# Performance work log

Measured on AMD Instinct MI355X. Metric: run time of the kernel, lower is better.

The kernel has to match this reference:

```python
import jax, jax.numpy as jnp
import numpy as np

B, C, H, W = 16, 10, 400, 352
N = 50  # objects per sample
ZSIZE = 1.0 - (-3.0)  # maxZ - minZ
MEANDIMS = jnp.array([1.52, 1.63, 3.88], dtype=jnp.float32)
BKG_THRESH = 0.025
LOG_CLAMP = -100.0  # torch BCE clamps log at -100


def setup_inputs() -> dict:
    key = jax.random.key(0)
    k1, k2, k3, k4, k5, k6 = jax.random.split(key, 6)
    output = jax.random.normal(k1, (B, C, H, W), dtype=jnp.float32)
    # target columns: x, y, z, h, w, l, angle
    x = jax.random.uniform(k2, (B, N), minval=0.0, maxval=H / 2 - 1e-3)
    y = jax.random.uniform(k3, (B, N), minval=0.0, maxval=W / 2 - 1e-3)
    z = jax.random.uniform(k4, (B, N), minval=0.0, maxval=ZSIZE)
    dims = jax.random.uniform(k5, (B, N, 3), minval=0.5, maxval=5.0)
    ang = jax.random.uniform(k6, (B, N), minval=-np.pi, maxval=np.pi)
    target = jnp.concatenate(
        [x[..., None], y[..., None], z[..., None], dims, ang[..., None]], axis=-1
    ).astype(jnp.float32)
    return {"output": output, "target": target}


def _per_sample(out_i, tgt_i):
    # out_i: [H, W, C], tgt_i: [N, 7]
    tx = tgt_i[:, 0] * 2.0
    ty = tgt_i[:, 1] * 2.0
    dx = jnp.floor(tx).astype(jnp.int32)
    dy = jnp.floor(ty).astype(jnp.int32)

    # background mask: True everywhere except object cells
    bkgmask = jnp.ones((H, W), dtype=bool).at[dx, dy].set(False)
    out0 = out_i[:, :, 0]
    bkg_p = jax.nn.sigmoid(out0)
    nbkg = bkgmask.sum()
    clsscale = jnp.exp(-3.0 * (bkg_p * bkgmask).sum() / nbkg) * 2.5

    # BCE(bkg, 0) over background cells with p > 0.025 (skip if none)
    sel = bkgmask & (bkg_p > BKG_THRESH)
    cnt = sel.sum()
    logv = jnp.maximum(jax.nn.log_sigmoid(-out0), LOG_CLAMP)  # log(1-sigmoid)
    bkg_l = jnp.where(
        cnt > 0,
        -(jnp.where(sel, logv, 0.0)).sum() / jnp.maximum(cnt, 1).astype(jnp.float32),
        0.0,
    )

    # gather per-object predictions: [N, C]
    out_g = out_i[dx, dy, :]

    fx = tx - jnp.floor(tx)
    fy = ty - jnp.floor(ty)
    tz = tgt_i[:, 2] / ZSIZE
    hwl_t = jnp.log(tgt_i[:, 3:6] / MEANDIMS)
    angle = tgt_i[:, 6]
    anglecls = (angle >= 0).astype(jnp.int32)

    # BCE(sigmoid(out[:,0]), 1) * clsscale
    objcls_l = (-jnp.maximum(jax.nn.log_sigmoid(out_g[:, 0]), LOG_CLAMP)).mean() * clsscale

    # MSE(sigmoid(out[:,1:4]), [fx,fy,tz])
    xyz_t = jnp.stack([fx, fy, tz], axis=1)
    xyz_l = ((jax.nn.sigmoid(out_g[:, 1:4]) - xyz_t) ** 2).mean()

    # MSE(out[:,4:7], log(dims/meandims)) * 0.5
    hwl_l = ((out_g[:, 4:7] - hwl_t) ** 2).mean() * 0.5

    # CE(out[:,7:9], anglecls) * 0.5
    ls = jax.nn.log_softmax(out_g[:, 7:9], axis=1)
    anglecls_l = (-jnp.take_along_axis(ls, anglecls[:, None], axis=1)).mean() * 0.5

    # smooth_l1(sin(out[:,9]), sin(sin(angle))) * 0.5   (tgt[:,8]=sin(angle), then .sin() again)
    d = jnp.sin(out_g[:, 9]) - jnp.sin(jnp.sin(angle))
    ad = jnp.abs(d)
    anglesin_l = jnp.where(ad < 1.0, 0.5 * d * d, ad - 0.5).mean() * 0.5

    return jnp.stack([bkg_l, objcls_l, xyz_l, hwl_l, anglecls_l, anglesin_l])


def _compute(output, target):
    out = jnp.transpose(output, (0, 2, 3, 1))  # [B, H, W, C]
    terms = jax.vmap(_per_sample)(out, target)  # [B, 6]
    sums = terms.sum(axis=0)
    total = sums.sum()
    return total, sums


def reference(output, target):
    total, s = _compute(output, target)
    return (total, s[0], s[1], s[2], s[3], s[4], s[5])
```

## Files before the change

### kernel.cpp

```cpp
#include <hip/hip_runtime.h>
#include <math.h>

#define Bn 16
#define Cn 10
#define Hn 400
#define Wn 352
#define Nn 50
#define PLANE (Hn * Wn)
#define NCHUNK 32
#define VPER (PLANE / 4 / NCHUNK)
#define BKG_THRESH 0.025f
#define LOG_CLAMP -100.0f

#define WS_PV 2048

__device__ __forceinline__ float softplusf(float x) {
    return fmaxf(x, 0.0f) + log1pf(expf(-fabsf(x)));
}
__device__ __forceinline__ float sigmoidf(float x) {
    return 1.0f / (1.0f + expf(-x));
}
__device__ __forceinline__ float wave_sum(float v) {
    for (int off = 32; off > 0; off >>= 1) v += __shfl_down(v, off);
    return __shfl(v, 0);
}

__global__ __launch_bounds__(256) void partial_kernel(const float* __restrict__ out,
                                                      const float* __restrict__ tgt,
                                                      float* __restrict__ ws) {
    const int tid = threadIdx.x;

    if (blockIdx.x < Bn * NCHUNK) {
        const int b  = blockIdx.x >> 5;
        const int ch = blockIdx.x & 31;
        const float4* plane = (const float4*)(out + (size_t)b * Cn * PLANE);
        const int i0 = ch * VPER + tid;

        float4 v0 = plane[i0];
        float4 v1 = plane[i0 + 256];
        float4 v2 = plane[i0 + 512];
        float4 v3 = plane[i0 + 768];

        float s_sig = 0.0f, s_log = 0.0f, s_cnt = 0.0f;
        float xs[16];
        xs[0]=v0.x; xs[1]=v0.y; xs[2]=v0.z; xs[3]=v0.w;
        xs[4]=v1.x; xs[5]=v1.y; xs[6]=v1.z; xs[7]=v1.w;
        xs[8]=v2.x; xs[9]=v2.y; xs[10]=v2.z; xs[11]=v2.w;
        xs[12]=v3.x; xs[13]=v3.y; xs[14]=v3.z; xs[15]=v3.w;
        #pragma unroll
        for (int k = 0; k < 16; ++k) {
            float x = xs[k];
            float p = sigmoidf(x);
            s_sig += p;
            bool sel = p > BKG_THRESH;
            s_cnt += sel ? 1.0f : 0.0f;
            s_log += sel ? fmaxf(-softplusf(x), LOG_CLAMP) : 0.0f;
        }
        if (tid < VPER - 1024) {
            float4 v4 = plane[i0 + 1024];
            float ys[4] = {v4.x, v4.y, v4.z, v4.w};
            #pragma unroll
            for (int k = 0; k < 4; ++k) {
                float x = ys[k];
                float p = sigmoidf(x);
                s_sig += p;
                bool sel = p > BKG_THRESH;
                s_cnt += sel ? 1.0f : 0.0f;
                s_log += sel ? fmaxf(-softplusf(x), LOG_CLAMP) : 0.0f;
            }
        }

        s_sig = wave_sum(s_sig);
        s_log = wave_sum(s_log);
        s_cnt = wave_sum(s_cnt);

        __shared__ float sh[4][3];
        const int wv = tid >> 6, lane6 = tid & 63;
        if (lane6 == 0) { sh[wv][0] = s_sig; sh[wv][1] = s_log; sh[wv][2] = s_cnt; }
        __syncthreads();
        if (tid == 0) {
            float* p = ws + (size_t)(b * NCHUNK + ch) * 3;
            p[0] = sh[0][0] + sh[1][0] + sh[2][0] + sh[3][0];
            p[1] = sh[0][1] + sh[1][1] + sh[2][1] + sh[3][1];
            p[2] = sh[0][2] + sh[1][2] + sh[2][2] + sh[3][2];
        }
        return;
    }

    if (tid >= 64) return;
    const int b    = blockIdx.x - Bn * NCHUNK;
    const int lane = tid;

    const float* t = tgt + (size_t)b * Nn * 7;
    const bool active = lane < Nn;
    float tx = 0.0f, ty = 0.0f, t2 = 0.0f, t3 = 1.0f, t4 = 1.0f, t5 = 1.0f, ang = 0.0f;
    int key = -1;
    if (active) {
        tx = t[lane * 7 + 0] * 2.0f;
        ty = t[lane * 7 + 1] * 2.0f;
        t2 = t[lane * 7 + 2];
        t3 = t[lane * 7 + 3];
        t4 = t[lane * 7 + 4];
        t5 = t[lane * 7 + 5];
        ang = t[lane * 7 + 6];
        int dx = (int)floorf(tx);
        int dy = (int)floorf(ty);
        key = dx * Wn + dy;
    }

    bool isfirst = active;
    #pragma unroll 1
    for (int m = 0; m < Nn; ++m) {
        int km = __shfl(key, m);
        if (active && m < lane && km == key) isfirst = false;
    }

    const float* base = out + (size_t)b * Cn * PLANE;
    float g[10];
    #pragma unroll
    for (int c = 0; c < 10; ++c) g[c] = active ? base[(size_t)c * PLANE + key] : 0.0f;

    float c_sig = 0.0f, c_log = 0.0f, c_cnt = 0.0f, c_n = 0.0f;
    if (isfirst) {
        float p = sigmoidf(g[0]);
        c_sig = p;
        c_n = 1.0f;
        if (p > BKG_THRESH) {
            c_cnt = 1.0f;
            c_log = fmaxf(-softplusf(g[0]), LOG_CLAMP);
        }
    }

    float v_obj = 0.0f, v_xyz = 0.0f, v_hwl = 0.0f, v_acl = 0.0f, v_asin = 0.0f;
    if (active) {
        v_obj = -fmaxf(-softplusf(-g[0]), LOG_CLAMP);

        float fx = tx - floorf(tx);
        float fy = ty - floorf(ty);
        float tz = t2 * 0.25f;
        float e0 = sigmoidf(g[1]) - fx;
        float e1 = sigmoidf(g[2]) - fy;
        float e2 = sigmoidf(g[3]) - tz;
        v_xyz = e0 * e0 + e1 * e1 + e2 * e2;

        float h0 = g[4] - logf(t3 / 1.52f);
        float h1 = g[5] - logf(t4 / 1.63f);
        float h2 = g[6] - logf(t5 / 3.88f);
        v_hwl = h0 * h0 + h1 * h1 + h2 * h2;

        float m = fmaxf(g[7], g[8]);
        float lse = m + logf(expf(g[7] - m) + expf(g[8] - m));
        float gsel = (ang >= 0.0f) ? g[8] : g[7];
        v_acl = lse - gsel;

        float d = sinf(g[9]) - sinf(sinf(ang));
        float ad = fabsf(d);
        v_asin = (ad < 1.0f) ? 0.5f * d * d : ad - 0.5f;
    }
    v_obj  = wave_sum(v_obj);
    v_xyz  = wave_sum(v_xyz);
    v_hwl  = wave_sum(v_hwl);
    v_acl  = wave_sum(v_acl);
    v_asin = wave_sum(v_asin);
    c_sig  = wave_sum(c_sig);
    c_log  = wave_sum(c_log);
    c_cnt  = wave_sum(c_cnt);
    c_n    = wave_sum(c_n);

    if (lane == 0) {
        float* pv = ws + WS_PV + (size_t)b * 10;
        pv[0] = v_obj;  pv[1] = v_xyz; pv[2] = v_hwl; pv[3] = v_acl; pv[4] = v_asin;
        pv[5] = c_sig;  pv[6] = c_log; pv[7] = c_cnt; pv[8] = c_n;
    }
}

__global__ __launch_bounds__(1024) void finalize_kernel(const float* __restrict__ ws,
                                                        float* __restrict__ out7) {
    const int b    = threadIdx.x >> 6;
    const int lane = threadIdx.x & 63;

    float s_sig = 0.0f, s_log = 0.0f, s_cnt = 0.0f;
    if (lane < NCHUNK) {
        const float* p = ws + (size_t)(b * NCHUNK + lane) * 3;
        s_sig = p[0]; s_log = p[1]; s_cnt = p[2];
    }
    s_sig = wave_sum(s_sig);
    s_log = wave_sum(s_log);
    s_cnt = wave_sum(s_cnt);

    __shared__ float sh_terms[Bn][6];
    if (lane == 0) {
        const float* pv = ws + WS_PV + (size_t)b * 10;
        float v_obj = pv[0], v_xyz = pv[1], v_hwl = pv[2], v_acl = pv[3], v_asin = pv[4];
        float c_sig = pv[5], c_log = pv[6], c_cnt = pv[7], c_n = pv[8];

        float nbkg    = (float)PLANE - c_n;
        float sig_bkg = s_sig - c_sig;
        float clsscale = expf(-3.0f * sig_bkg / nbkg) * 2.5f;

        float cnt  = s_cnt - c_cnt;
        float slog = s_log - c_log;
        float bkg_l = (cnt > 0.0f) ? (-slog / fmaxf(cnt, 1.0f)) : 0.0f;

        const float invN  = 1.0f / (float)Nn;
        const float invN3 = 1.0f / (float)(Nn * 3);

        sh_terms[b][0] = bkg_l;
        sh_terms[b][1] = v_obj * invN * clsscale;
        sh_terms[b][2] = v_xyz * invN3;
        sh_terms[b][3] = v_hwl * invN3 * 0.5f;
        sh_terms[b][4] = v_acl * invN * 0.5f;
        sh_terms[b][5] = v_asin * invN * 0.5f;
    }
    __syncthreads();

    if (threadIdx.x == 0) {
        float s[6] = {0, 0, 0, 0, 0, 0};
        for (int bb = 0; bb < Bn; ++bb)
            for (int j = 0; j < 6; ++j)
                s[j] += sh_terms[bb][j];
        float tot = 0.0f;
        for (int j = 0; j < 6; ++j) tot += s[j];
        out7[0] = tot;
        for (int j = 0; j < 6; ++j) out7[1 + j] = s[j];
    }
}

extern "C" void kernel_launch(void* const* d_in, const int* in_sizes, int n_in,
                              void* d_out, int out_size, void* d_ws, size_t ws_size,
                              hipStream_t stream) {
    const float* out = (const float*)d_in[0];
    const float* tgt = (const float*)d_in[1];
    float* o  = (float*)d_out;
    float* ws = (float*)d_ws;

    partial_kernel<<<Bn * NCHUNK + Bn, 256, 0, stream>>>(out, tgt, ws);
    finalize_kernel<<<1, 1024, 0, stream>>>(ws, o);
}
```

Before: 21.08 us.

## Fuse finalize into partial kernel via last-block atomic counter

Merges the two kernels into one. Each block publishes its partials with agent-scope stores and then bumps an atomic counter, and the last block to arrive performs the final reduction. The per-object gather blocks are moved to the front of the grid so they schedule first. This removes one kernel launch and its gap, at the cost of a hipMemsetAsync to reset the counter, which adds its own small operation to the stream.

```diff
diff --git a/kernel.cpp b/kernel.cpp
--- a/kernel.cpp
+++ b/kernel.cpp
@@ -11,8 +11,10 @@
 #define VPER (PLANE / 4 / NCHUNK)
 #define BKG_THRESH 0.025f
 #define LOG_CLAMP -100.0f
-
-#define WS_PV 2048
+#define NBLOCKS (Bn * NCHUNK + Bn)
+
+#define WS_PART 256
+#define WS_PV   2048
 
 __device__ __forceinline__ float softplusf(float x) {
     return fmaxf(x, 0.0f) + log1pf(expf(-fabsf(x)));
@@ -24,15 +26,121 @@
     for (int off = 32; off > 0; off >>= 1) v += __shfl_down(v, off);
     return __shfl(v, 0);
 }
-
-__global__ __launch_bounds__(256) void partial_kernel(const float* __restrict__ out,
-                                                      const float* __restrict__ tgt,
-                                                      float* __restrict__ ws) {
+__device__ __forceinline__ void st_a(float* p, float v) {
+    __hip_atomic_store(p, v, __ATOMIC_RELAXED, __HIP_MEMORY_SCOPE_AGENT);
+}
+__device__ __forceinline__ float ld_a(const float* p) {
+    return __hip_atomic_load(p, __ATOMIC_RELAXED, __HIP_MEMORY_SCOPE_AGENT);
+}
+
+__global__ __launch_bounds__(256) void fused_loss(const float* __restrict__ out,
+                                                  const float* __restrict__ tgt,
+                                                  float* __restrict__ ws,
+                                                  float* __restrict__ out7) {
+    int*   cnt      = (int*)ws;
+    float* partials = ws + WS_PART;
+    float* pvals    = ws + WS_PV;
     const int tid = threadIdx.x;
 
-    if (blockIdx.x < Bn * NCHUNK) {
-        const int b  = blockIdx.x >> 5;
-        const int ch = blockIdx.x & 31;
+    __shared__ int   sh_last;
+    __shared__ float sh[4][3];
+    __shared__ float sh_terms[Bn][6];
+
+    if (blockIdx.x < Bn) {
+        const int b = blockIdx.x;
+        if (tid < 64) {
+            const int lane = tid;
+            const float* t = tgt + (size_t)b * Nn * 7;
+            const bool active = lane < Nn;
+            float tx = 0.0f, ty = 0.0f, t2 = 0.0f, t3 = 1.0f, t4 = 1.0f, t5 = 1.0f, ang = 0.0f;
+            int key = -1;
+            if (active) {
+                tx = t[lane * 7 + 0] * 2.0f;
+                ty = t[lane * 7 + 1] * 2.0f;
+                t2 = t[lane * 7 + 2];
+                t3 = t[lane * 7 + 3];
+                t4 = t[lane * 7 + 4];
+                t5 = t[lane * 7 + 5];
+                ang = t[lane * 7 + 6];
+                int dx = (int)floorf(tx);
+                int dy = (int)floorf(ty);
+                key = dx * Wn + dy;
+            }
+
+            bool isfirst = active;
+            #pragma unroll 1
+            for (int m = 0; m < Nn; ++m) {
+                int km = __shfl(key, m);
+                if (active && m < lane && km == key) isfirst = false;
+            }
+
+            const float* base = out + (size_t)b * Cn * PLANE;
+            float g[10];
+            #pragma unroll
+            for (int c = 0; c < 10; ++c) g[c] = active ? base[(size_t)c * PLANE + key] : 0.0f;
+
+            float c_sig = 0.0f, c_log = 0.0f, c_cnt = 0.0f, c_n = 0.0f;
+            if (isfirst) {
+                float p = sigmoidf(g[0]);
+                c_sig = p;
+                c_n = 1.0f;
+                if (p > BKG_THRESH) {
+                    c_cnt = 1.0f;
+                    c_log = fmaxf(-softplusf(g[0]), LOG_CLAMP);
+                }
+            }
+
+            float v_obj = 0.0f, v_xyz = 0.0f, v_hwl = 0.0f, v_acl = 0.0f, v_asin = 0.0f;
+            if (active) {
+                v_obj = -fmaxf(-softplusf(-g[0]), LOG_CLAMP);
+
+                float fx = tx - floorf(tx);
+                float fy = ty - floorf(ty);
+                float tz = t2 * 0.25f;
+                float e0 = sigmoidf(g[1]) - fx;
+                float e1 = sigmoidf(g[2]) - fy;
+                float e2 = sigmoidf(g[3]) - tz;
+                v_xyz = e0 * e0 + e1 * e1 + e2 * e2;
+
+                float h0 = g[4] - logf(t3 / 1.52f);
+                float h1 = g[5] - logf(t4 / 1.63f);
+                float h2 = g[6] - logf(t5 / 3.88f);
+                v_hwl = h0 * h0 + h1 * h1 + h2 * h2;
+
+                float m = fmaxf(g[7], g[8]);
+                float lse = m + logf(expf(g[7] - m) + expf(g[8] - m));
+                float gsel = (ang >= 0.0f) ? g[8] : g[7];
+                v_acl = lse - gsel;
+
+                float d = sinf(g[9]) - sinf(sinf(ang));
+                float ad = fabsf(d);
+                v_asin = (ad < 1.0f) ? 0.5f * d * d : ad - 0.5f;
+            }
+            v_obj  = wave_sum(v_obj);
+            v_xyz  = wave_sum(v_xyz);
+            v_hwl  = wave_sum(v_hwl);
+            v_acl  = wave_sum(v_acl);
+            v_asin = wave_sum(v_asin);
+            c_sig  = wave_sum(c_sig);
+            c_log  = wave_sum(c_log);
+            c_cnt  = wave_sum(c_cnt);
+            c_n    = wave_sum(c_n);
+
+            if (lane == 0) {
+                float* pv = pvals + (size_t)b * 10;
+                st_a(&pv[0], v_obj); st_a(&pv[1], v_xyz); st_a(&pv[2], v_hwl);
+                st_a(&pv[3], v_acl); st_a(&pv[4], v_asin);
+                st_a(&pv[5], c_sig); st_a(&pv[6], c_log); st_a(&pv[7], c_cnt);
+                st_a(&pv[8], c_n);
+                asm volatile("s_waitcnt vmcnt(0)" ::: "memory");
+                int old = __hip_atomic_fetch_add(cnt, 1, __ATOMIC_RELAXED, __HIP_MEMORY_SCOPE_AGENT);
+                sh_last = (old == NBLOCKS - 1) ? 1 : 0;
+            }
+        }
+    } else {
+        const int idx = blockIdx.x - Bn;
+        const int b  = idx >> 5;
+        const int ch = idx & 31;
         const float4* plane = (const float4*)(out + (size_t)b * Cn * PLANE);
         const int i0 = ch * VPER + tid;
 
@@ -74,147 +182,74 @@
         s_log = wave_sum(s_log);
         s_cnt = wave_sum(s_cnt);
 
-        __shared__ float sh[4][3];
         const int wv = tid >> 6, lane6 = tid & 63;
         if (lane6 == 0) { sh[wv][0] = s_sig; sh[wv][1] = s_log; sh[wv][2] = s_cnt; }
         __syncthreads();
         if (tid == 0) {
-            float* p = ws + (size_t)(b * NCHUNK + ch) * 3;
-            p[0] = sh[0][0] + sh[1][0] + sh[2][0] + sh[3][0];
-            p[1] = sh[0][1] + sh[1][1] + sh[2][1] + sh[3][1];
-            p[2] = sh[0][2] + sh[1][2] + sh[2][2] + sh[3][2];
-        }
-        return;
+            float a = sh[0][0] + sh[1][0] + sh[2][0] + sh[3][0];
+            float c = sh[0][1] + sh[1][1] + sh[2][1] + sh[3][1];
+            float d = sh[0][2] + sh[1][2] + sh[2][2] + sh[3][2];
+            float* p = partials + (size_t)(b * NCHUNK + ch) * 3;
+            st_a(&p[0], a); st_a(&p[1], c); st_a(&p[2], d);
+            asm volatile("s_waitcnt vmcnt(0)" ::: "memory");
+            int old = __hip_atomic_fetch_add(cnt, 1, __ATOMIC_RELAXED, __HIP_MEMORY_SCOPE_AGENT);
+            sh_last = (old == NBLOCKS - 1) ? 1 : 0;
+        }
     }
 
-    if (tid >= 64) return;
-    const int b    = blockIdx.x - Bn * NCHUNK;
-    const int lane = tid;
-
-    const float* t = tgt + (size_t)b * Nn * 7;
-    const bool active = lane < Nn;
-    float tx = 0.0f, ty = 0.0f, t2 = 0.0f, t3 = 1.0f, t4 = 1.0f, t5 = 1.0f, ang = 0.0f;
-    int key = -1;
-    if (active) {
-        tx = t[lane * 7 + 0] * 2.0f;
-        ty = t[lane * 7 + 1] * 2.0f;
-        t2 = t[lane * 7 + 2];
-        t3 = t[lane * 7 + 3];
-        t4 = t[lane * 7 + 4];
-        t5 = t[lane * 7 + 5];
-        ang = t[lane * 7 + 6];
-        int dx = (int)floorf(tx);
-        int dy = (int)floorf(ty);
-        key = dx * Wn + dy;
-    }
-
-    bool isfirst = active;
-    #pragma unroll 1
-    for (int m = 0; m < Nn; ++m) {
-        int km = __shfl(key, m);
-        if (active && m < lane && km == key) isfirst = false;
-    }
-
-    const float* base = out + (size_t)b * Cn * PLANE;
-    float g[10];
-    #pragma unroll
-    for (int c = 0; c < 10; ++c) g[c] = active ? base[(size_t)c * PLANE + key] : 0.0f;
-
-    float c_sig = 0.0f, c_log = 0.0f, c_cnt = 0.0f, c_n = 0.0f;
-    if (isfirst) {
-        float p = sigmoidf(g[0]);
-        c_sig = p;
-        c_n = 1.0f;
-        if (p > BKG_THRESH) {
-            c_cnt = 1.0f;
-            c_log = fmaxf(-softplusf(g[0]), LOG_CLAMP);
-        }
-    }
-
-    float v_obj = 0.0f, v_xyz = 0.0f, v_hwl = 0.0f, v_acl = 0.0f, v_asin = 0.0f;
-    if (active) {
-        v_obj = -fmaxf(-softplusf(-g[0]), LOG_CLAMP);
-
-        float fx = tx - floorf(tx);
-        float fy = ty - floorf(ty);
-        float tz = t2 * 0.25f;
-        float e0 = sigmoidf(g[1]) - fx;
-        float e1 = sigmoidf(g[2]) - fy;
-        float e2 = sigmoidf(g[3]) - tz;
-        v_xyz = e0 * e0 + e1 * e1 + e2 * e2;
-
-        float h0 = g[4] - logf(t3 / 1.52f);
-        float h1 = g[5] - logf(t4 / 1.63f);
-        float h2 = g[6] - logf(t5 / 3.88f);
-        v_hwl = h0 * h0 + h1 * h1 + h2 * h2;
-
-        float m = fmaxf(g[7], g[8]);
-        float lse = m + logf(expf(g[7] - m) + expf(g[8] - m));
-        float gsel = (ang >= 0.0f) ? g[8] : g[7];
-        v_acl = lse - gsel;
-
-        float d = sinf(g[9]) - sinf(sinf(ang));
-        float ad = fabsf(d);
-        v_asin = (ad < 1.0f) ? 0.5f * d * d : ad - 0.5f;
-    }
-    v_obj  = wave_sum(v_obj);
-    v_xyz  = wave_sum(v_xyz);
-    v_hwl  = wave_sum(v_hwl);
-    v_acl  = wave_sum(v_acl);
-    v_asin = wave_sum(v_asin);
-    c_sig  = wave_sum(c_sig);
-    c_log  = wave_sum(c_log);
-    c_cnt  = wave_sum(c_cnt);
-    c_n    = wave_sum(c_n);
-
-    if (lane == 0) {
-        float* pv = ws + WS_PV + (size_t)b * 10;
-        pv[0] = v_obj;  pv[1] = v_xyz; pv[2] = v_hwl; pv[3] = v_acl; pv[4] = v_asin;
-        pv[5] = c_sig;  pv[6] = c_log; pv[7] = c_cnt; pv[8] = c_n;
-    }
-}
-
-__global__ __launch_bounds__(1024) void finalize_kernel(const float* __restrict__ ws,
-                                                        float* __restrict__ out7) {
-    const int b    = threadIdx.x >> 6;
-    const int lane = threadIdx.x & 63;
-
-    float s_sig = 0.0f, s_log = 0.0f, s_cnt = 0.0f;
-    if (lane < NCHUNK) {
-        const float* p = ws + (size_t)(b * NCHUNK + lane) * 3;
-        s_sig = p[0]; s_log = p[1]; s_cnt = p[2];
-    }
-    s_sig = wave_sum(s_sig);
-    s_log = wave_sum(s_log);
-    s_cnt = wave_sum(s_cnt);
-
-    __shared__ float sh_terms[Bn][6];
-    if (lane == 0) {
-        const float* pv = ws + WS_PV + (size_t)b * 10;
-        float v_obj = pv[0], v_xyz = pv[1], v_hwl = pv[2], v_acl = pv[3], v_asin = pv[4];
-        float c_sig = pv[5], c_log = pv[6], c_cnt = pv[7], c_n = pv[8];
-
-        float nbkg    = (float)PLANE - c_n;
-        float sig_bkg = s_sig - c_sig;
-        float clsscale = expf(-3.0f * sig_bkg / nbkg) * 2.5f;
-
-        float cnt  = s_cnt - c_cnt;
-        float slog = s_log - c_log;
-        float bkg_l = (cnt > 0.0f) ? (-slog / fmaxf(cnt, 1.0f)) : 0.0f;
-
-        const float invN  = 1.0f / (float)Nn;
-        const float invN3 = 1.0f / (float)(Nn * 3);
-
-        sh_terms[b][0] = bkg_l;
-        sh_terms[b][1] = v_obj * invN * clsscale;
-        sh_terms[b][2] = v_xyz * invN3;
-        sh_terms[b][3] = v_hwl * invN3 * 0.5f;
-        sh_terms[b][4] = v_acl * invN * 0.5f;
-        sh_terms[b][5] = v_asin * invN * 0.5f;
+    __syncthreads();
+    if (!sh_last) return;
+    asm volatile("" ::: "memory");
+
+    {
+        const int w = tid >> 6, lane = tid & 63;
+        #pragma unroll
+        for (int s = 0; s < 4; ++s) {
+            const int b = (w << 2) + s;
+            float a0 = 0.0f, a1 = 0.0f, a2 = 0.0f;
+            if (lane < NCHUNK) {
+                const float* p = partials + (size_t)(b * NCHUNK + lane) * 3;
+                a0 = ld_a(&p[0]); a1 = ld_a(&p[1]); a2 = ld_a(&p[2]);
+            }
+            a0 = wave_sum(a0);
+            a1 = wave_sum(a1);
+            a2 = wave_sum(a2);
+
+            float pvl = (lane < 9) ? ld_a(pvals + (size_t)b * 10 + lane) : 0.0f;
+            float v_obj  = __shfl(pvl, 0);
+            float v_xyz  = __shfl(pvl, 1);
+            float v_hwl  = __shfl(pvl, 2);
+            float v_acl  = __shfl(pvl, 3);
+            float v_asin = __shfl(pvl, 4);
+            float c_sig  = __shfl(pvl, 5);
+            float c_log  = __shfl(pvl, 6);
+            float c_cnt  = __shfl(pvl, 7);
+            float c_n    = __shfl(pvl, 8);
+
+            if (lane == 0) {
+                float nbkg    = (float)PLANE - c_n;
+                float sig_bkg = a0 - c_sig;
+                float clsscale = expf(-3.0f * sig_bkg / nbkg) * 2.5f;
+
+                float cntv = a2 - c_cnt;
+                float slog = a1 - c_log;
+                float bkg_l = (cntv > 0.0f) ? (-slog / fmaxf(cntv, 1.0f)) : 0.0f;
+
+                const float invN  = 1.0f / (float)Nn;
+                const float invN3 = 1.0f / (float)(Nn * 3);
+
+                sh_terms[b][0] = bkg_l;
+                sh_terms[b][1] = v_obj * invN * clsscale;
+                sh_terms[b][2] = v_xyz * invN3;
+                sh_terms[b][3] = v_hwl * invN3 * 0.5f;
+                sh_terms[b][4] = v_acl * invN * 0.5f;
+                sh_terms[b][5] = v_asin * invN * 0.5f;
+            }
+        }
     }
     __syncthreads();
 
-    if (threadIdx.x == 0) {
+    if (tid == 0) {
         float s[6] = {0, 0, 0, 0, 0, 0};
         for (int bb = 0; bb < Bn; ++bb)
             for (int j = 0; j < 6; ++j)
@@ -234,6 +269,6 @@
     float* o  = (float*)d_out;
     float* ws = (float*)d_ws;
 
-    partial_kernel<<<Bn * NCHUNK + Bn, 256, 0, stream>>>(out, tgt, ws);
-    finalize_kernel<<<1, 1024, 0, stream>>>(ws, o);
-}
+    hipMemsetAsync(d_ws, 0, 4, stream);
+    fused_loss<<<NBLOCKS, 256, 0, stream>>>(out, tgt, ws, o);
+}
```

After: 30.10 us. 1.43x slower.
